# Optimization experiments

Hardware: AMD Instinct MI355X
Metric: run time of the kernel (lower is better)

## Reference

```python
import jax, jax.numpy as jnp
import numpy as np

B, N, D_FEAT = 16, 1024, 64
NPOINT, RADIUS, NSAMPLE = 512, 0.2, 32
EPS = 1e-5


def _square_distance(src, dst):
    # src [b,S,3], dst [b,N,3] -> [b,S,N]
    d = -2.0 * jnp.einsum('bsc,bnc->bsn', src, dst)
    d = d + jnp.sum(src * src, -1)[:, :, None]
    d = d + jnp.sum(dst * dst, -1)[:, None, :]
    return d


def _fps(xyz, npoint):
    # xyz [b,N,3] -> indices [b,npoint]; seeded by point farthest from the mean
    b, n, _ = xyz.shape
    centroid = jnp.mean(xyz, axis=1, keepdims=True)
    distance = jnp.minimum(jnp.full((b, n), 1e10, xyz.dtype),
                           jnp.sum((xyz - centroid) ** 2, -1))
    farthest = jnp.argmax(distance, -1)
    bidx = jnp.arange(b)

    def body(carry, _):
        dist, far = carry
        c = xyz[bidx[:, None], far[:, None]]  # [b,1,3]
        dist = jnp.minimum(dist, jnp.sum((xyz - c) ** 2, -1))
        return (dist, jnp.argmax(dist, -1)), far

    _, idx = jax.lax.scan(body, (distance, farthest), None, length=npoint)
    return idx.T  # [b, npoint]


def _gather(points, idx):
    # points [b,N,C], idx [b,...] -> [b,...,C]
    return jax.vmap(lambda p, i: p[i])(points, idx)


def _query_ball(radius, nsample, xyz, new_xyz):
    # faithful to torch: mask out-of-radius with N, full sort, take first nsample,
    # replace sentinels by the first (closest-index) in-ball point
    b, n, _ = xyz.shape
    sqr = _square_distance(new_xyz, xyz)  # [b,S,N]
    idx = jnp.where(sqr > radius ** 2, n, jnp.arange(n)[None, None, :])
    idx = jnp.sort(idx, axis=-1)[:, :, :nsample]
    first = idx[:, :, :1]
    return jnp.where(idx == n, first, idx)


def _qbn(x):
    # QBN_RM training mode: divide by per-channel RMS of detached activations
    mean = jnp.mean(jax.lax.stop_gradient(x) ** 2, axis=(0, 2, 3))
    return x / jnp.sqrt(mean + EPS)[None, :, None, None]


def _qrelu(x):
    # scale each 3-vector by mod / max(mod, 1), coefficient detached
    b3, c, s, k = x.shape
    b = b3 // 3
    xd = jax.lax.stop_gradient(x).reshape(b, 3, c, s, k)
    mod = jnp.sqrt(jnp.sum(xd * xd, axis=1))  # [b,c,s,k]
    coeff = mod / jnp.maximum(mod, 1.0)
    return jnp.broadcast_to(coeff[:, None], (b, 3, c, s, k)).reshape(b3, c, s, k) * x


def _qmaxpool(x):
    # our_mpool1d with kernel (1, nsample): pick the max-modulus sample over K,
    # gather the same index for all 3 quaternion components
    b3, c, s, k = x.shape
    b = b3 // 3
    x5 = x.reshape(b, 3, c, s, k)
    mod = jnp.sum(jax.lax.stop_gradient(x5) ** 2, axis=1)  # argmax of mod == argmax of mod^2
    idx = jnp.argmax(mod, axis=-1)  # [b,c,s]
    idxb = jnp.broadcast_to(idx[:, None, :, :, None], (b, 3, c, s, 1))
    y = jnp.take_along_axis(x5, idxb, axis=-1)[..., 0]  # [b,3,c,s]
    return y.reshape(b3, c, s)


def setup_inputs() -> dict:
    key = jax.random.key(0)
    k1, k2, k3, k4, k5 = jax.random.split(key, 5)
    xyz = jax.random.normal(k1, (B, 3, N), dtype=jnp.float32)
    points = jax.random.normal(k2, (B * 3, D_FEAT, N), dtype=jnp.float32)
    W0 = jax.random.normal(k3, (64, 66), dtype=jnp.float32) * np.sqrt(2.0 / 66)
    W1 = jax.random.normal(k4, (64, 64), dtype=jnp.float32) * np.sqrt(2.0 / 64)
    W2 = jax.random.normal(k5, (128, 64), dtype=jnp.float32) * np.sqrt(2.0 / 64)
    return {"xyz": xyz, "points": points, "W0": W0, "W1": W1, "W2": W2}


def reference(xyz, points, W0, W1, W2):
    xyz_t = xyz.transpose(0, 2, 1)      # [B,N,3]
    pts_t = points.transpose(0, 2, 1)   # [B*3,N,D]

    fps_idx = _fps(xyz_t, NPOINT)                       # [B,S]
    new_xyz = _gather(xyz_t, fps_idx)                   # [B,S,3]
    idx = _query_ball(RADIUS, NSAMPLE, xyz_t, new_xyz)  # [B,S,K]

    g_xyz = _gather(xyz_t, idx)                         # [B,S,K,3]
    g_norm = g_xyz - new_xyz[:, :, None, :]
    gx = g_xyz.transpose(0, 3, 1, 2).reshape(B * 3, NPOINT, NSAMPLE, 1)
    gn = g_norm.transpose(0, 3, 1, 2).reshape(B * 3, NPOINT, NSAMPLE, 1)
    idx3 = jnp.broadcast_to(idx[:, None], (B, 3, NPOINT, NSAMPLE)).reshape(B * 3, NPOINT, NSAMPLE)
    gp = _gather(pts_t, idx3)                           # [B*3,S,K,D]

    x = jnp.concatenate([gn, gx, gp], axis=-1)          # [B*3,S,K,D+2]
    x = x.transpose(0, 3, 1, 2)                         # [B*3,D+2,S,K]
    for W in (W0, W1, W2):
        x = jnp.einsum('bcsk,oc->bosk', x, W)           # 1x1 conv, no bias
        x = _qrelu(_qbn(x))
    new_feat = _qmaxpool(x)                             # [B*3,128,S]
    return new_xyz.transpose(0, 2, 1), new_feat
```

## Files before the change

kernel.cpp:

```cpp
#include <hip/hip_runtime.h>

typedef unsigned int u32;

#define NB 16
#define NPT 1024
#define NP 512
#define NS 32
#define DF 64
#define RAD2 0.04f
#define EPSQ 1e-5f
#define CNTF 786432.0f
#define NGRP 8192
#define TCAP 96
#define TSLOT 128
#define NTILE_MAX 2731

__device__ __forceinline__ float rmul(float a, float b){ return __fmul_rn(a,b); }
__device__ __forceinline__ float radd(float a, float b){ return __fadd_rn(a,b); }
__device__ __forceinline__ float sq3(float a, float b, float c){
  return radd(radd(rmul(a,a), rmul(b,b)), rmul(c,c));
}

__device__ __forceinline__ float wave_sum64(float v){
  #pragma unroll
  for(int m=1;m<64;m<<=1) v += __shfl_xor(v, m, 64);
  return v;
}

#define DPPCOMB(CTRL) do{ \
  float _ov = __int_as_float(__builtin_amdgcn_mov_dpp(__float_as_int(m), (CTRL), 0xF, 0xF, true)); \
  int   _oi = __builtin_amdgcn_mov_dpp(mi, (CTRL), 0xF, 0xF, true); \
  if(_ov > m || (_ov == m && _oi < mi)){ m = _ov; mi = _oi; } \
}while(0)

__device__ __forceinline__ int wave_argmax1024(const float* dist, int lane){
  float v8[8]; int j8[8];
  #pragma unroll
  for(int q=0;q<8;q++){
    float l = dist[q], r = dist[q+8];
    bool tk = (r > l);
    v8[q] = tk ? r : l; j8[q] = tk ? q+8 : q;
  }
  float v4[4]; int j4[4];
  #pragma unroll
  for(int q=0;q<4;q++){
    bool tk = (v8[q+4] > v8[q]);
    v4[q] = tk ? v8[q+4] : v8[q]; j4[q] = tk ? j8[q+4] : j8[q];
  }
  float v2[2]; int j2[2];
  #pragma unroll
  for(int q=0;q<2;q++){
    bool tk = (v4[q+2] > v4[q]);
    v2[q] = tk ? v4[q+2] : v4[q]; j2[q] = tk ? j4[q+2] : j4[q];
  }
  bool tk = (v2[1] > v2[0]);
  float m = tk ? v2[1] : v2[0];
  int mi = lane*16 + (tk ? j2[1] : j2[0]);
  DPPCOMB(0xB1);
  DPPCOMB(0x4E);
  DPPCOMB(0x124);
  DPPCOMB(0x128);
  DPPCOMB(0x142);
  DPPCOMB(0x143);
  return __builtin_amdgcn_readlane(mi, 63);
}

template<int PT>
__global__ __launch_bounds__(256) void fps_combo(const float* __restrict__ xyz,
                                                 float* __restrict__ out0,
                                                 const float* __restrict__ pts,
                                                 float* __restrict__ ptsT,
                                                 u32* __restrict__ witem){
  const int bid = blockIdx.x;
  const int t = threadIdx.x;
  if(bid >= NB){
    const int gid = (bid - NB)*256 + t;
    if(gid < NTILE_MAX*TSLOT) witem[gid] = 0xFFFFFFFFu;
    if constexpr(PT){
      const int w = gid >> 6, ln = gid & 63;
      if(w < 48*16){
        const int b3 = w >> 4, n0 = (w & 15) << 6;
        const float* src = pts + (((size_t)b3*64 + ln) << 10);
        float* dst = ptsT + (((size_t)b3*1024 + n0) << 6) + ln;
        #pragma unroll 4
        for(int i=0;i<64;i++) dst[(size_t)i << 6] = src[n0 + i];
      }
    }
    return;
  }
  if(t >= 64) return;
  const int lane = t;
  const int b = bid;
  const float* xb = xyz + b*3*NPT;
  float px[16], py[16], pz[16], dist[16];
  #pragma unroll
  for(int j=0;j<16;j++){
    const int n = lane*16 + j;
    px[j] = xb[n]; py[j] = xb[NPT+n]; pz[j] = xb[2*NPT+n];
  }
  float sx=0.f, sy=0.f, sz=0.f;
  #pragma unroll
  for(int j=0;j<16;j++){ sx+=px[j]; sy+=py[j]; sz+=pz[j]; }
  sx = wave_sum64(sx); sy = wave_sum64(sy); sz = wave_sum64(sz);
  const float cx = sx/1024.f, cy = sy/1024.f, cz = sz/1024.f;
  #pragma unroll
  for(int j=0;j<16;j++){
    float dx = px[j]-cx, dy = py[j]-cy, dz = pz[j]-cz;
    dist[j] = fminf(1e10f, sq3(dx,dy,dz));
  }
  int far = wave_argmax1024(dist, lane);
  for(int it=0; it<NP; ++it){
    const float qx = xb[far], qy = xb[NPT+far], qz = xb[2*NPT+far];
    if(lane == 0){
      out0[(b*3+0)*NP + it] = qx;
      out0[(b*3+1)*NP + it] = qy;
      out0[(b*3+2)*NP + it] = qz;
    }
    #pragma unroll
    for(int j=0;j<16;j++){
      float dx = px[j]-qx, dy = py[j]-qy, dz = pz[j]-qz;
      float nd = sq3(dx,dy,dz);
      dist[j] = fminf(dist[j], nd);
    }
    far = wave_argmax1024(dist, lane);
  }
}

__global__ __launch_bounds__(256) void ball_kernel(const float* __restrict__ xyz,
                                                   const float* __restrict__ out0,
                                                   int* __restrict__ idxb,
                                                   int* __restrict__ cntb){
  const int gw = (blockIdx.x * 256 + threadIdx.x) >> 6;
  const int lane = threadIdx.x & 63;
  const int b = gw >> 9;
  const int s = gw & 511;
  const float s0 = out0[(b*3+0)*NP + s];
  const float s1 = out0[(b*3+1)*NP + s];
  const float s2 = out0[(b*3+2)*NP + s];
  const float ss = sq3(s0,s1,s2);
  const float* xb = xyz + b*3*NPT;
  int base = 0;
  int* row = idxb + (b*NP + s)*NS;
  for(int chk=0; chk<16 && base<NS; ++chk){
    const int n = chk*64 + lane;
    float d0 = xb[n], d1 = xb[NPT+n], d2 = xb[2*NPT+n];
    float dd = sq3(d0,d1,d2);
    float p  = radd(radd(rmul(s0,d0), rmul(s1,d1)), rmul(s2,d2));
    float sqr = radd(radd(rmul(-2.0f,p), ss), dd);
    bool inc = !(sqr > RAD2);
    unsigned long long mask = __ballot(inc);
    if(inc){
      int slot = base + __popcll(mask & ((1ull<<lane)-1ull));
      if(slot < NS) row[slot] = n;
    }
    base += __popcll(mask);
  }
  if(lane==0) cntb[gw] = (base < NS) ? base : NS;
}

__global__ __launch_bounds__(1024) void pack_kernel(const int* __restrict__ cntb,
                                                    const int* __restrict__ idxb,
                                                    u32* __restrict__ witem,
                                                    int* __restrict__ ntile_dev){
  const int t = threadIdx.x;
  const int lane = t & 63;
  const int wv = t >> 6;
  int c[8]; int s0 = 0;
  #pragma unroll
  for(int i=0;i<8;i++){ c[i] = cntb[t*8+i]; s0 += c[i]; }
  int pre = s0;
  #pragma unroll
  for(int d=1; d<64; d<<=1){
    int v = __shfl_up(pre, d, 64);
    if(lane >= d) pre += v;
  }
  __shared__ int wsum[16];
  if(lane==63) wsum[wv] = pre;
  __syncthreads();
  int wo = 0;
  #pragma unroll
  for(int w=0;w<16;w++) if(w < wv) wo += wsum[w];
  int m = wo + pre - s0;
  if(t==1023) *ntile_dev = (wo + pre + TCAP - 1) / TCAP;
  #pragma unroll
  for(int i=0;i<8;i++){
    const int g = t*8+i; const int cc = c[i];
    const int tile = m / TCAP; const int slot = m - TCAP*tile;
    const int* row = idxb + g*NS;
    for(int j=0;j<cc;j++){
      witem[tile*TSLOT + slot + j] = (u32)((g<<15) | (j<<10) | row[j]);
    }
    m += cc;
  }
}

template<int DEPTH, int PT>
__global__ __launch_bounds__(384) void pass_kernel(
  const float* __restrict__ xyz, const float* __restrict__ ptsrc,
  const float* __restrict__ W0, const float* __restrict__ W1, const float* __restrict__ W2,
  const float* __restrict__ out0, const u32* __restrict__ witem,
  const int* __restrict__ cntb, const int* __restrict__ ntile_dev,
  const float* __restrict__ inv1, const float* __restrict__ inv2,
  float* __restrict__ part, float* __restrict__ out1)
{
  const int t = threadIdx.x;
  const int c3 = t >> 7;
  const int r  = t & 127;
  const int lane = t & 63;
  const int wv = t >> 6;
  const int bi = blockIdx.x;

  if(bi >= *ntile_dev) return;

  __shared__ float sq[3][128][17];
  __shared__ float wstat[6][128];
  for(int i=t; i<6*128; i+=384) (&wstat[0][0])[i] = 0.f;
  __syncthreads();

  const u32 w = witem[bi*TSLOT + r];
  const bool valid = (w != 0xFFFFFFFFu);
  const int bs = valid ? (int)(w >> 15) : 0;
  const int j  = valid ? (int)((w >> 10) & 31) : 1;
  const int n  = valid ? (int)(w & 1023) : 0;
  const int b = bs >> 9;
  const int s = bs & 511;
  const int b3 = b*3 + c3;
  const int cv = cntb[bs];
  const float wgt = valid ? ((j==0) ? (float)(33 - cv) : 1.0f) : 0.0f;

  const float gx = xyz[b3*NPT + n];
  const float cx = out0[b3*NP + s];
  float x0[66];
  x0[0] = gx - cx;
  x0[1] = gx;
  if constexpr(PT){
    const float4* pr4 = reinterpret_cast<const float4*>(ptsrc + (((size_t)b3<<10) + (size_t)n)*DF);
    #pragma unroll
    for(int q=0;q<16;q++){
      float4 v = pr4[q];
      x0[2+4*q] = v.x; x0[3+4*q] = v.y; x0[4+4*q] = v.z; x0[5+4*q] = v.w;
    }
  } else {
    const float* pr = ptsrc + ((size_t)b3*DF)*NPT + n;
    #pragma unroll
    for(int c=0;c<DF;c++) x0[2+c] = pr[(size_t)c*NPT];
  }

  float y1[64];
  #pragma unroll
  for(int ch=0; ch<4; ++ch){
    float acc[16];
    #pragma unroll
    for(int oo=0;oo<16;oo++){
      const int o = ch*16+oo;
      float a = 0.f;
      #pragma unroll
      for(int c=0;c<66;c++) a = fmaf(W0[o*66+c], x0[c], a);
      acc[oo] = a;
    }
    if constexpr(DEPTH == 1){
      #pragma unroll
      for(int oo=0;oo<16;oo++){
        float v = wave_sum64(acc[oo]*acc[oo]*wgt);
        if(lane==0) wstat[wv][ch*16+oo] += v;
      }
    } else {
      #pragma unroll
      for(int oo=0;oo<16;oo++){
        const int o = ch*16+oo;
        float xp = acc[oo] * inv1[o];
        acc[oo] = xp;
        sq[c3][r][oo] = xp*xp;
      }
      __syncthreads();
      #pragma unroll
      for(int oo=0;oo<16;oo++){
        float m2 = (sq[0][r][oo] + sq[1][r][oo]) + sq[2][r][oo];
        float mod = sqrtf(m2);
        float cf = (mod >= 1.f) ? 1.f : mod;
        y1[ch*16+oo] = cf * acc[oo];
      }
      __syncthreads();
    }
  }
  if constexpr(DEPTH == 1){
    __syncthreads();
    if(t < 64){
      float sv = 0.f;
      #pragma unroll
      for(int wq=0;wq<6;wq++) sv += wstat[wq][t];
      part[bi*64 + t] = sv;
    }
    return;
  }

  float y2[64];
  #pragma unroll
  for(int ch=0; ch<4; ++ch){
    float acc[16];
    #pragma unroll
    for(int oo=0;oo<16;oo++){
      const int o = ch*16+oo;
      float a = 0.f;
      #pragma unroll
      for(int c=0;c<64;c++) a = fmaf(W1[o*64+c], y1[c], a);
      acc[oo] = a;
    }
    if constexpr(DEPTH == 2){
      #pragma unroll
      for(int oo=0;oo<16;oo++){
        float v = wave_sum64(acc[oo]*acc[oo]*wgt);
        if(lane==0) wstat[wv][ch*16+oo] += v;
      }
    } else {
      #pragma unroll
      for(int oo=0;oo<16;oo++){
        const int o = ch*16+oo;
        float xp = acc[oo] * inv2[o];
        acc[oo] = xp;
        sq[c3][r][oo] = xp*xp;
      }
      __syncthreads();
      #pragma unroll
      for(int oo=0;oo<16;oo++){
        float m2 = (sq[0][r][oo] + sq[1][r][oo]) + sq[2][r][oo];
        float mod = sqrtf(m2);
        float cf = (mod >= 1.f) ? 1.f : mod;
        y2[ch*16+oo] = cf * acc[oo];
      }
      __syncthreads();
    }
  }
  if constexpr(DEPTH == 2){
    __syncthreads();
    if(t < 64){
      float sv = 0.f;
      #pragma unroll
      for(int wq=0;wq<6;wq++) sv += wstat[wq][t];
      part[bi*64 + t] = sv;
    }
    return;
  }

  #pragma unroll
  for(int ch=0; ch<8; ++ch){
    float a3[16];
    #pragma unroll
    for(int oo=0;oo<16;oo++){
      const int o = ch*16+oo;
      float a = 0.f;
      #pragma unroll
      for(int c=0;c<64;c++) a = fmaf(W2[o*64+c], y2[c], a);
      a3[oo] = a;
      sq[c3][r][oo] = a;
    }
    __syncthreads();
    if(c3 == 0){
      #pragma unroll
      for(int oo=0;oo<16;oo++){
        float a0 = sq[0][r][oo], a1 = sq[1][r][oo], a2 = sq[2][r][oo];
        float m2 = radd(radd(rmul(a0,a0), rmul(a1,a1)), rmul(a2,a2));
        float v = wave_sum64(m2*wgt);
        if(lane==0) wstat[wv][ch*16+oo] += v;
        if(valid && j==0){
          float bvv = m2; int bjj = 0;
          for(int jj=1; jj<cv; ++jj){
            float c0 = sq[0][r+jj][oo], c1 = sq[1][r+jj][oo], c2 = sq[2][r+jj][oo];
            float mm = radd(radd(rmul(c0,c0), rmul(c1,c1)), rmul(c2,c2));
            if(mm > bvv){ bvv = mm; bjj = jj; }
          }
          const int o = ch*16+oo;
          #pragma unroll
          for(int cc=0;cc<3;cc++){
            out1[(((size_t)(3*b+cc))*128 + o)*NP + s] = sq[cc][r+bjj][oo];
          }
        }
      }
    }
    __syncthreads();
  }
  if(t < 128){
    part[bi*128 + t] = wstat[0][t] + wstat[1][t];
  }
}

__global__ __launch_bounds__(256) void fin_kernel(const float* __restrict__ part,
                                                  const int* __restrict__ ntile_dev, int nch,
                                                  float* __restrict__ inv){
  const int o = blockIdx.x;
  const int t = threadIdx.x;
  const int nblk = *ntile_dev;
  float sum = 0.f;
  for(int i=t; i<nblk; i+=256) sum += part[(size_t)i*nch + o];
  sum = wave_sum64(sum);
  __shared__ float red[4];
  if((t&63)==0) red[t>>6] = sum;
  __syncthreads();
  if(t==0){
    float tot = (red[0]+red[1])+(red[2]+red[3]);
    inv[o] = 1.0f / sqrtf(tot/CNTF + EPSQ);
  }
}

__global__ __launch_bounds__(256) void fin3_scale(const float* __restrict__ part3,
                                                  const int* __restrict__ ntile_dev,
                                                  float* __restrict__ out){
  const int o = blockIdx.x;
  const int t = threadIdx.x;
  const int nblk = *ntile_dev;
  float sum = 0.f;
  for(int i=t; i<nblk; i+=256) sum += part3[(size_t)i*128 + o];
  sum = wave_sum64(sum);
  __shared__ float red[4];
  __shared__ float sinv;
  if((t&63)==0) red[t>>6] = sum;
  __syncthreads();
  if(t==0){
    float tot = (red[0]+red[1])+(red[2]+red[3]);
    sinv = 1.0f / sqrtf(tot/CNTF + EPSQ);
  }
  __syncthreads();
  const float iv = sinv;
  float* base = out + NB*3*NP;
  const size_t str = (size_t)128*NP;
  for(int idx=t; idx<NB*NP; idx+=256){
    const int b = idx >> 9, s = idx & 511;
    size_t i0 = ((size_t)(b*3)*128 + o)*NP + s;
    float a0 = base[i0] * iv;
    float a1 = base[i0+str] * iv;
    float a2 = base[i0+2*str] * iv;
    float m2 = (a0*a0 + a1*a1) + a2*a2;
    float mod = sqrtf(m2);
    float cf = (mod >= 1.f) ? 1.f : mod;
    base[i0] = cf*a0; base[i0+str] = cf*a1; base[i0+2*str] = cf*a2;
  }
}

extern "C" void kernel_launch(void* const* d_in, const int* in_sizes, int n_in,
                              void* d_out, int out_size, void* d_ws, size_t ws_size,
                              hipStream_t stream){
  const float* xyz = (const float*)d_in[0];
  const float* pts = (const float*)d_in[1];
  const float* W0  = (const float*)d_in[2];
  const float* W1  = (const float*)d_in[3];
  const float* W2  = (const float*)d_in[4];
  float* out = (float*)d_out;

  char* p = (char*)d_ws;
  auto carve = [&](size_t bytes)->char*{
    char* q = p; p += (bytes + 255) & ~(size_t)255; return q;
  };
  int*   idxb      = (int*)  carve((size_t)NGRP*NS*4);
  int*   cntb      = (int*)  carve((size_t)NGRP*4);
  u32*   witem     = (u32*)  carve((size_t)NTILE_MAX*TSLOT*4);
  int*   ntile_dev = (int*)  carve(256);
  float* part1     = (float*)carve((size_t)NTILE_MAX*64*4);
  float* part2     = (float*)carve((size_t)NTILE_MAX*64*4);
  float* part3     = (float*)carve((size_t)NTILE_MAX*128*4);
  float* inv1      = (float*)carve(64*4);
  float* inv2      = (float*)carve(64*4);
  float* inv3      = (float*)carve(128*4);
  size_t base_need = (size_t)(p - (char*)d_ws);
  float* ptsT      = (float*)p;
  const size_t pt_bytes = (size_t)48*1024*64*4;
  const bool use_pt = (ws_size >= base_need + pt_bytes);

  float* out1 = out + NB*3*NP;

  const int copyblk = (NTILE_MAX*TSLOT + 255)/256;
  if(use_pt) fps_combo<1><<<NB + copyblk, 256, 0, stream>>>(xyz, out, pts, ptsT, witem);
  else       fps_combo<0><<<NB + copyblk, 256, 0, stream>>>(xyz, out, pts, nullptr, witem);

  ball_kernel<<<2048, 256, 0, stream>>>(xyz, out, idxb, cntb);
  pack_kernel<<<1, 1024, 0, stream>>>(cntb, idxb, witem, ntile_dev);

  if(use_pt){
    pass_kernel<1,1><<<NTILE_MAX, 384, 0, stream>>>(xyz, ptsT, W0, W1, W2, out, witem, cntb, ntile_dev, nullptr, nullptr, part1, nullptr);
    fin_kernel<<<64, 256, 0, stream>>>(part1, ntile_dev, 64, inv1);
    pass_kernel<2,1><<<NTILE_MAX, 384, 0, stream>>>(xyz, ptsT, W0, W1, W2, out, witem, cntb, ntile_dev, inv1, nullptr, part2, nullptr);
    fin_kernel<<<64, 256, 0, stream>>>(part2, ntile_dev, 64, inv2);
    pass_kernel<3,1><<<NTILE_MAX, 384, 0, stream>>>(xyz, ptsT, W0, W1, W2, out, witem, cntb, ntile_dev, inv1, inv2, part3, out1);
  } else {
    pass_kernel<1,0><<<NTILE_MAX, 384, 0, stream>>>(xyz, pts, W0, W1, W2, out, witem, cntb, ntile_dev, nullptr, nullptr, part1, nullptr);
    fin_kernel<<<64, 256, 0, stream>>>(part1, ntile_dev, 64, inv1);
    pass_kernel<2,0><<<NTILE_MAX, 384, 0, stream>>>(xyz, pts, W0, W1, W2, out, witem, cntb, ntile_dev, inv1, nullptr, part2, nullptr);
    fin_kernel<<<64, 256, 0, stream>>>(part2, ntile_dev, 64, inv2);
    pass_kernel<3,0><<<NTILE_MAX, 384, 0, stream>>>(xyz, pts, W0, W1, W2, out, witem, cntb, ntile_dev, inv1, inv2, part3, out1);
  }
  fin3_scale<<<128, 256, 0, stream>>>(part3, ntile_dev, out);
}
```

Measured before the change: 830.6 us.

## Pack two FPS batches per wave with packed-float math and 64-bit key argmax

The farthest-point-sampling loop now runs two batches per wavefront, one per 32-lane half, using packed float2 arithmetic for the distance updates. The argmax packs the distance and an inverted index into one 64-bit key, so each reduction step is a single compare. The query point is read from LDS rather than global memory. The serial 512-step FPS chain is the critical path, and this aims to shorten each step while halving the number of FPS blocks. Risks are a longer per-step dependency chain on two batches and extra register pressure.

```diff
diff --git a/kernel.cpp b/kernel.cpp
--- a/kernel.cpp
+++ b/kernel.cpp
@@ -1,6 +1,8 @@
 #include <hip/hip_runtime.h>
 
 typedef unsigned int u32;
+typedef unsigned long long u64;
+typedef float v2f __attribute__((ext_vector_type(2)));
 
 #define NB 16
 #define NPT 1024
@@ -27,43 +29,19 @@
   return v;
 }
 
-#define DPPCOMB(CTRL) do{ \
-  float _ov = __int_as_float(__builtin_amdgcn_mov_dpp(__float_as_int(m), (CTRL), 0xF, 0xF, true)); \
-  int   _oi = __builtin_amdgcn_mov_dpp(mi, (CTRL), 0xF, 0xF, true); \
-  if(_ov > m || (_ov == m && _oi < mi)){ m = _ov; mi = _oi; } \
+__device__ __forceinline__ float half_sum32(float v){
+  #pragma unroll
+  for(int m=1;m<32;m<<=1) v += __shfl_xor(v, m, 64);
+  return v;
+}
+
+#define DPPK(CTRL) do{ \
+  unsigned _lo = (unsigned)k, _hi = (unsigned)(k>>32); \
+  unsigned _mlo = (unsigned)__builtin_amdgcn_mov_dpp((int)_lo, (CTRL), 0xF, 0xF, true); \
+  unsigned _mhi = (unsigned)__builtin_amdgcn_mov_dpp((int)_hi, (CTRL), 0xF, 0xF, true); \
+  u64 _mk = ((u64)_mhi<<32) | _mlo; \
+  k = (_mk > k) ? _mk : k; \
 }while(0)
-
-__device__ __forceinline__ int wave_argmax1024(const float* dist, int lane){
-  float v8[8]; int j8[8];
-  #pragma unroll
-  for(int q=0;q<8;q++){
-    float l = dist[q], r = dist[q+8];
-    bool tk = (r > l);
-    v8[q] = tk ? r : l; j8[q] = tk ? q+8 : q;
-  }
-  float v4[4]; int j4[4];
-  #pragma unroll
-  for(int q=0;q<4;q++){
-    bool tk = (v8[q+4] > v8[q]);
-    v4[q] = tk ? v8[q+4] : v8[q]; j4[q] = tk ? j8[q+4] : j8[q];
-  }
-  float v2[2]; int j2[2];
-  #pragma unroll
-  for(int q=0;q<2;q++){
-    bool tk = (v4[q+2] > v4[q]);
-    v2[q] = tk ? v4[q+2] : v4[q]; j2[q] = tk ? j4[q+2] : j4[q];
-  }
-  bool tk = (v2[1] > v2[0]);
-  float m = tk ? v2[1] : v2[0];
-  int mi = lane*16 + (tk ? j2[1] : j2[0]);
-  DPPCOMB(0xB1);
-  DPPCOMB(0x4E);
-  DPPCOMB(0x124);
-  DPPCOMB(0x128);
-  DPPCOMB(0x142);
-  DPPCOMB(0x143);
-  return __builtin_amdgcn_readlane(mi, 63);
-}
 
 template<int PT>
 __global__ __launch_bounds__(256) void fps_combo(const float* __restrict__ xyz,
@@ -71,10 +49,11 @@
                                                  const float* __restrict__ pts,
                                                  float* __restrict__ ptsT,
                                                  u32* __restrict__ witem){
+#pragma clang fp contract(off)
   const int bid = blockIdx.x;
   const int t = threadIdx.x;
-  if(bid >= NB){
-    const int gid = (bid - NB)*256 + t;
+  if(bid >= 8){
+    const int gid = (bid - 8)*256 + t;
     if(gid < NTILE_MAX*TSLOT) witem[gid] = 0xFFFFFFFFu;
     if constexpr(PT){
       const int w = gid >> 6, ln = gid & 63;
@@ -88,41 +67,100 @@
     }
     return;
   }
+  __shared__ float4 plds[2048];
   if(t >= 64) return;
   const int lane = t;
-  const int b = bid;
+  const int half = lane >> 5;
+  const int hl   = lane & 31;
+  const int b    = 2*bid + half;
   const float* xb = xyz + b*3*NPT;
-  float px[16], py[16], pz[16], dist[16];
-  #pragma unroll
-  for(int j=0;j<16;j++){
-    const int n = lane*16 + j;
-    px[j] = xb[n]; py[j] = xb[NPT+n]; pz[j] = xb[2*NPT+n];
+
+  v2f px2[16], py2[16], pz2[16], dist2[16];
+  u32 loj[32];
+  #pragma unroll
+  for(int i=0;i<16;i++){
+    const int n0 = 64*i + hl, n1 = n0 + 32;
+    float x0v = xb[n0],        x1v = xb[n1];
+    float y0v = xb[NPT+n0],    y1v = xb[NPT+n1];
+    float z0v = xb[2*NPT+n0],  z1v = xb[2*NPT+n1];
+    px2[i].x = x0v; px2[i].y = x1v;
+    py2[i].x = y0v; py2[i].y = y1v;
+    pz2[i].x = z0v; pz2[i].y = z1v;
+    loj[2*i]   = 1023u - (u32)n0;
+    loj[2*i+1] = 1023u - (u32)n1;
+    plds[(half<<10) + n0] = make_float4(x0v, y0v, z0v, 0.f);
+    plds[(half<<10) + n1] = make_float4(x1v, y1v, z1v, 0.f);
   }
   float sx=0.f, sy=0.f, sz=0.f;
   #pragma unroll
-  for(int j=0;j<16;j++){ sx+=px[j]; sy+=py[j]; sz+=pz[j]; }
-  sx = wave_sum64(sx); sy = wave_sum64(sy); sz = wave_sum64(sz);
+  for(int i=0;i<16;i++){
+    sx += px2[i].x; sx += px2[i].y;
+    sy += py2[i].x; sy += py2[i].y;
+    sz += pz2[i].x; sz += pz2[i].y;
+  }
+  sx = half_sum32(sx); sy = half_sum32(sy); sz = half_sum32(sz);
   const float cx = sx/1024.f, cy = sy/1024.f, cz = sz/1024.f;
-  #pragma unroll
-  for(int j=0;j<16;j++){
-    float dx = px[j]-cx, dy = py[j]-cy, dz = pz[j]-cz;
-    dist[j] = fminf(1e10f, sq3(dx,dy,dz));
-  }
-  int far = wave_argmax1024(dist, lane);
+  {
+    v2f cx2; cx2.x=cx; cx2.y=cx;
+    v2f cy2; cy2.x=cy; cy2.y=cy;
+    v2f cz2; cz2.x=cz; cz2.y=cz;
+    #pragma unroll
+    for(int i=0;i<16;i++){
+      v2f dx = px2[i]-cx2, dy = py2[i]-cy2, dz = pz2[i]-cz2;
+      v2f m1 = dx*dx, m2 = dy*dy, a1 = m1+m2, m3 = dz*dz, s2 = a1+m3;
+      dist2[i].x = fminf(1e10f, s2.x);
+      dist2[i].y = fminf(1e10f, s2.y);
+    }
+  }
+  auto reduce2 = [&](int& fA, int& fB){
+    u64 kk[16];
+    #pragma unroll
+    for(int i=0;i<16;i++){
+      float a = dist2[i].x, bb = dist2[i].y;
+      bool tk = bb > a;
+      float dw = tk ? bb : a;
+      u32   lw = tk ? loj[2*i+1] : loj[2*i];
+      kk[i] = ((u64)__float_as_uint(dw)<<32) | lw;
+    }
+    #pragma unroll
+    for(int i=0;i<8;i++){ u64 l=kk[2*i], r=kk[2*i+1]; kk[i] = (r>l)?r:l; }
+    #pragma unroll
+    for(int i=0;i<4;i++){ u64 l=kk[2*i], r=kk[2*i+1]; kk[i] = (r>l)?r:l; }
+    #pragma unroll
+    for(int i=0;i<2;i++){ u64 l=kk[2*i], r=kk[2*i+1]; kk[i] = (r>l)?r:l; }
+    u64 k = (kk[1]>kk[0]) ? kk[1] : kk[0];
+    DPPK(0xB1);
+    DPPK(0x4E);
+    DPPK(0x124);
+    DPPK(0x128);
+    DPPK(0x142);
+    unsigned lo = (unsigned)k;
+    fA = 1023 - __builtin_amdgcn_readlane((int)lo, 31);
+    fB = 1023 - __builtin_amdgcn_readlane((int)lo, 63);
+  };
+
+  __asm__ volatile("s_waitcnt lgkmcnt(0)" ::: "memory");
+  int farA, farB;
+  reduce2(farA, farB);
   for(int it=0; it<NP; ++it){
-    const float qx = xb[far], qy = xb[NPT+far], qz = xb[2*NPT+far];
-    if(lane == 0){
-      out0[(b*3+0)*NP + it] = qx;
-      out0[(b*3+1)*NP + it] = qy;
-      out0[(b*3+2)*NP + it] = qz;
-    }
-    #pragma unroll
-    for(int j=0;j<16;j++){
-      float dx = px[j]-qx, dy = py[j]-qy, dz = pz[j]-qz;
-      float nd = sq3(dx,dy,dz);
-      dist[j] = fminf(dist[j], nd);
-    }
-    far = wave_argmax1024(dist, lane);
+    const int farv = (lane & 32) ? farB : farA;
+    const float4 qv = plds[(half<<10) + farv];
+    if(hl == 0){
+      out0[(b*3+0)*NP + it] = qv.x;
+      out0[(b*3+1)*NP + it] = qv.y;
+      out0[(b*3+2)*NP + it] = qv.z;
+    }
+    v2f qx2; qx2.x=qv.x; qx2.y=qv.x;
+    v2f qy2; qy2.x=qv.y; qy2.y=qv.y;
+    v2f qz2; qz2.x=qv.z; qz2.y=qv.z;
+    #pragma unroll
+    for(int i=0;i<16;i++){
+      v2f dx = px2[i]-qx2, dy = py2[i]-qy2, dz = pz2[i]-qz2;
+      v2f m1 = dx*dx, m2 = dy*dy, a1 = m1+m2, m3 = dz*dz, s2 = a1+m3;
+      dist2[i].x = fminf(dist2[i].x, s2.x);
+      dist2[i].y = fminf(dist2[i].y, s2.y);
+    }
+    reduce2(farA, farB);
   }
 }
 
@@ -468,8 +506,8 @@
   float* out1 = out + NB*3*NP;
 
   const int copyblk = (NTILE_MAX*TSLOT + 255)/256;
-  if(use_pt) fps_combo<1><<<NB + copyblk, 256, 0, stream>>>(xyz, out, pts, ptsT, witem);
-  else       fps_combo<0><<<NB + copyblk, 256, 0, stream>>>(xyz, out, pts, nullptr, witem);
+  if(use_pt) fps_combo<1><<<8 + copyblk, 256, 0, stream>>>(xyz, out, pts, ptsT, witem);
+  else       fps_combo<0><<<8 + copyblk, 256, 0, stream>>>(xyz, out, pts, nullptr, witem);
 
   ball_kernel<<<2048, 256, 0, stream>>>(xyz, out, idxb, cntb);
   pack_kernel<<<1, 1024, 0, stream>>>(cntb, idxb, witem, ntile_dev);
```

Result: faster. 777.7 us (-6.4%).
